# Performance work log

Measured on AMD Instinct MI355X. Metric: run time of the kernel, lower is better.

## Reference

```python
import jax, jax.numpy as jnp
import numpy as np

B, L, DIM = 1, 2048, 4096
H, KV, HD = 32, 8, 128
REP = H // KV
SCALE = HD ** -0.5
ROPE_BASE = 10000.0


def rope_traditional(x, offset=0):
    # x: [B, H, L, D] ; traditional RoPE rotates interleaved pairs (x[2i], x[2i+1])
    D = x.shape[-1]
    Lx = x.shape[2]
    pos = jnp.arange(offset, offset + Lx, dtype=jnp.float32)            # [L]
    inv_freq = ROPE_BASE ** (-jnp.arange(0, D, 2, dtype=jnp.float32) / D)  # [D/2]
    ang = pos[:, None] * inv_freq[None, :]                               # [L, D/2]
    c, s = jnp.cos(ang), jnp.sin(ang)
    x1 = x[..., 0::2]
    x2 = x[..., 1::2]
    r1 = x1 * c - x2 * s
    r2 = x1 * s + x2 * c
    return jnp.stack([r1, r2], axis=-1).reshape(x.shape).astype(x.dtype)


def setup_inputs() -> dict:
    key = jax.random.key(0)
    k0, k1, k2, k3, k4 = jax.random.split(key, 5)
    x = jax.random.normal(k0, (B, L, DIM), dtype=jnp.float32)
    wq = jax.random.normal(k1, (DIM, H * HD), dtype=jnp.float32) * 0.02
    wk = jax.random.normal(k2, (DIM, KV * HD), dtype=jnp.float32) * 0.02
    wv = jax.random.normal(k3, (DIM, KV * HD), dtype=jnp.float32) * 0.02
    wo = jax.random.normal(k4, (H * HD, DIM), dtype=jnp.float32) * 0.02
    # additive causal mask (prefill)
    causal = jnp.tril(jnp.ones((L, L), dtype=bool))
    mask = jnp.where(causal, 0.0, -1e9).astype(jnp.float32)
    return {"x": x, "wq": wq, "wk": wk, "wv": wv, "wo": wo, "mask": mask}


def reference(x, wq, wk, wv, wo, mask):
    Bx, Lx, _ = x.shape
    q = (x @ wq).reshape(Bx, Lx, H, HD).transpose(0, 2, 1, 3)   # [B,H,L,hd]
    k = (x @ wk).reshape(Bx, Lx, KV, HD).transpose(0, 2, 1, 3)  # [B,KV,L,hd]
    v = (x @ wv).reshape(Bx, Lx, KV, HD).transpose(0, 2, 1, 3)
    # GQA head repeat (each kv head repeated REP times contiguously)
    k = jnp.repeat(k, REP, axis=1)  # [B,H,L,hd]
    v = jnp.repeat(v, REP, axis=1)
    # RoPE applied after repeat (cache=None branch), offset 0
    q = rope_traditional(q)
    k = rope_traditional(k)
    scores = jnp.einsum("bhld,bhmd->bhlm", q * SCALE, k) + mask  # [B,H,L,L]
    probs = jax.nn.softmax(scores.astype(jnp.float32), axis=-1).astype(scores.dtype)
    out = jnp.einsum("bhlm,bhmd->bhld", probs, v)
    out = out.transpose(0, 2, 1, 3).reshape(Bx, Lx, H * HD)
    return out @ wo, k, v
```

## Files before the change

### kernel.cpp

```cpp
#include <hip/hip_runtime.h>
#include <hip/hip_bf16.h>
#include <math.h>


#define L_SEQ 2048
#define DIM   4096
#define NH    32
#define NKV   8
#define HD    128
#define SCALE 0.08838834764831845f

typedef __bf16 bf16x8 __attribute__((ext_vector_type(8)));
typedef __bf16 bf16x4 __attribute__((ext_vector_type(4)));
typedef __bf16 bf16x2 __attribute__((ext_vector_type(2)));
typedef float  f32x4  __attribute__((ext_vector_type(4)));

__device__ __forceinline__ void gld16(const void* g, void* l) {
  __builtin_amdgcn_global_load_lds(
      (const __attribute__((address_space(1))) void*)g,
      (__attribute__((address_space(3))) void*)l, 16, 0, 0);
}

__global__ void cast_bf16_kernel(const float* __restrict__ in,
                                 __bf16* __restrict__ out, long n4) {
  long i = blockIdx.x * (long)blockDim.x + threadIdx.x;
  if (i >= n4) return;
  float4 f = reinterpret_cast<const float4*>(in)[i];
  bf16x4 o;
  o[0] = (__bf16)f.x; o[1] = (__bf16)f.y; o[2] = (__bf16)f.z; o[3] = (__bf16)f.w;
  reinterpret_cast<bf16x4*>(out)[i] = o;
}

__global__ void tcast_kernel(const float* __restrict__ in0, __bf16* __restrict__ out0,
                             const float* __restrict__ in1, __bf16* __restrict__ out1,
                             int K, int N) {
  __shared__ float tile[32][33];
  const float* in  = blockIdx.z ? in1  : in0;
  __bf16*     out  = blockIdx.z ? out1 : out0;
  int n0 = blockIdx.x * 32, k0 = blockIdx.y * 32;
  int tx = threadIdx.x & 31, ty = threadIdx.x >> 5;
#pragma unroll
  for (int i = 0; i < 4; ++i)
    tile[ty + i * 8][tx] = in[(long)(k0 + ty + i * 8) * N + n0 + tx];
  __syncthreads();
#pragma unroll
  for (int i = 0; i < 4; ++i)
    out[(long)(n0 + ty + i * 8) * K + k0 + tx] = (__bf16)tile[tx][ty + i * 8];
}

template<int TN>
__global__ __launch_bounds__(512, 2) void gemm_t(
    const __bf16* __restrict__ A, const __bf16* __restrict__ B0,
    const __bf16* __restrict__ B1, void* __restrict__ C0, void* __restrict__ C1,
    int M, int N, int K, int mode) {
  constexpr int ABY = 128 * 64 * 2;
  constexpr int BBY = TN * 64 * 2;
  constexpr int BUF = ABY + BBY;
  __shared__ char lds[3 * BUF] __attribute__((aligned(16)));
  const __bf16* Bt = blockIdx.z ? B1 : B0;
  void* C = blockIdx.z ? C1 : C0;

  const int nwg = gridDim.x * gridDim.y;
  const int bid = blockIdx.y * gridDim.x + blockIdx.x;
  const int swz = (bid & 7) * (nwg >> 3) + (bid >> 3);
  const int n0 = (swz % gridDim.x) * TN;
  const int m0 = (swz / gridDim.x) * 128;

  const int t = threadIdx.x, wave = t >> 6, lane = t & 63;
  const int quad = lane >> 4, l16 = lane & 15;
  const int wm = (wave >> 2) * 64, wn = (wave & 3) * (TN / 4);

  const int srow = t >> 3;
  const int scol = ((t & 7) ^ (srow & 7)) * 8;
  const __bf16* pa = A  + (long)(m0 + srow) * K + scol;
  const __bf16* pb = Bt + (long)(n0 + srow) * K + scol;
  const long K64 = (long)64 * K;
  const int ldsA = wave * 1024;
  const int ldsB = ABY + wave * 1024;

  int aoff[2][4], boff[2][TN / 64];
#pragma unroll
  for (int ks = 0; ks < 2; ++ks) {
    const int sw = ((ks * 4 + quad) ^ (l16 & 7)) * 16;
#pragma unroll
    for (int i = 0; i < 4; ++i)
      aoff[ks][i] = (wm + i * 16 + l16) * 128 + sw;
#pragma unroll
    for (int i = 0; i < TN / 64; ++i)
      boff[ks][i] = ABY + (wn + i * 16 + l16) * 128 + sw;
  }

  f32x4 acc[4][TN / 64] = {};
  const int nt = K >> 6;

  {
    char* bb = lds;
#pragma unroll
    for (int pt = 0; pt < 2; ++pt) {
#pragma unroll
      for (int r = 0; r < 2; ++r) gld16(pa + r * K64, bb + ldsA + r * 8192);
#pragma unroll
      for (int r = 0; r < TN / 64; ++r) gld16(pb + r * K64, bb + ldsB + r * 8192);
      pa += 64; pb += 64;
      bb += BUF;
    }
  }

  char* cb = lds;
  char* sb = lds + 2 * BUF;

#pragma unroll 1
  for (int kt = 0; kt < nt - 1; ++kt) {
    if constexpr (TN == 256) asm volatile("s_waitcnt vmcnt(6)" ::: "memory");
    else                     asm volatile("s_waitcnt vmcnt(4)" ::: "memory");
    __builtin_amdgcn_s_barrier();
    bf16x8 af[4], bfr[TN / 64];
#pragma unroll
    for (int i = 0; i < 4; ++i) af[i] = *(const bf16x8*)(cb + aoff[0][i]);
#pragma unroll
    for (int i = 0; i < TN / 64; ++i) bfr[i] = *(const bf16x8*)(cb + boff[0][i]);
    if (kt + 2 < nt) {
#pragma unroll
      for (int r = 0; r < 2; ++r) gld16(pa + r * K64, sb + ldsA + r * 8192);
#pragma unroll
      for (int r = 0; r < TN / 64; ++r) gld16(pb + r * K64, sb + ldsB + r * 8192);
      pa += 64; pb += 64;
    }
    __builtin_amdgcn_s_setprio(1);
#pragma unroll
    for (int tm = 0; tm < 4; ++tm)
#pragma unroll
      for (int tn = 0; tn < TN / 64; ++tn)
        acc[tm][tn] = __builtin_amdgcn_mfma_f32_16x16x32_bf16(
            af[tm], bfr[tn], acc[tm][tn], 0, 0, 0);
    __builtin_amdgcn_s_setprio(0);
#pragma unroll
    for (int i = 0; i < 4; ++i) af[i] = *(const bf16x8*)(cb + aoff[1][i]);
#pragma unroll
    for (int i = 0; i < TN / 64; ++i) bfr[i] = *(const bf16x8*)(cb + boff[1][i]);
    __builtin_amdgcn_s_setprio(1);
#pragma unroll
    for (int tm = 0; tm < 4; ++tm)
#pragma unroll
      for (int tn = 0; tn < TN / 64; ++tn)
        acc[tm][tn] = __builtin_amdgcn_mfma_f32_16x16x32_bf16(
            af[tm], bfr[tn], acc[tm][tn], 0, 0, 0);
    __builtin_amdgcn_s_setprio(0);
    cb += BUF; if (cb == lds + 3 * BUF) cb = lds;
    sb += BUF; if (sb == lds + 3 * BUF) sb = lds;
  }

  asm volatile("s_waitcnt vmcnt(0)" ::: "memory");
  __builtin_amdgcn_s_barrier();
  {
    bf16x8 af[4], bfr[TN / 64];
#pragma unroll
    for (int ks = 0; ks < 2; ++ks) {
#pragma unroll
      for (int i = 0; i < 4; ++i) af[i] = *(const bf16x8*)(cb + aoff[ks][i]);
#pragma unroll
      for (int i = 0; i < TN / 64; ++i) bfr[i] = *(const bf16x8*)(cb + boff[ks][i]);
      __builtin_amdgcn_s_setprio(1);
#pragma unroll
      for (int tm = 0; tm < 4; ++tm)
#pragma unroll
        for (int tn = 0; tn < TN / 64; ++tn)
          acc[tm][tn] = __builtin_amdgcn_mfma_f32_16x16x32_bf16(
              af[tm], bfr[tn], acc[tm][tn], 0, 0, 0);
      __builtin_amdgcn_s_setprio(0);
    }
  }

#pragma unroll
  for (int tm = 0; tm < 4; ++tm)
#pragma unroll
    for (int tn = 0; tn < TN / 64; ++tn)
#pragma unroll
      for (int r = 0; r < 4; ++r) {
        int row = m0 + wm + tm * 16 + quad * 4 + r;
        int col = n0 + wn + tn * 16 + l16;
        float v = acc[tm][tn][r];
        if (mode == 0) {
          ((float*)C)[(long)row * N + col] = v;
        } else {
          long idx = ((long)(col >> 7) * L_SEQ + row) * HD + (col & 127);
          ((__bf16*)C)[idx] = (__bf16)v;
        }
      }
}

#define NLOG2_10K 13.287712379549449f

__global__ void rope_q_kernel(__bf16* __restrict__ q ) {
  int idx = blockIdx.x * blockDim.x + threadIdx.x;
  int i = idx & 63, l = (idx >> 6) & 2047, h = idx >> 17;
  if (h >= NH) return;
  long base = ((long)h * L_SEQ + l) * HD + 2 * i;
  bf16x2 x12 = *(bf16x2*)(q + base);
  float x1 = (float)x12[0], x2 = (float)x12[1];
  float inv = exp2f((float)i * (-NLOG2_10K / 64.0f));
  float s, c; __sincosf((float)l * inv, &s, &c);
  bf16x2 o; o[0] = (__bf16)(x1 * c - x2 * s); o[1] = (__bf16)(x1 * s + x2 * c);
  *(bf16x2*)(q + base) = o;
}

__global__ void ropekv_kernel(__bf16* __restrict__ kb ,
                              const __bf16* __restrict__ vb,
                              float* __restrict__ kout ,
                              float* __restrict__ vout) {
  int idx = blockIdx.x * blockDim.x + threadIdx.x;
  int i = idx & 63, l = (idx >> 6) & 2047, kv = idx >> 17;
  if (kv >= NKV) return;
  long base = ((long)kv * L_SEQ + l) * HD + 2 * i;
  bf16x2 x12 = *(bf16x2*)(kb + base);
  float x1 = (float)x12[0], x2 = (float)x12[1];
  float inv = exp2f((float)i * (-NLOG2_10K / 64.0f));
  float s, c; __sincosf((float)l * inv, &s, &c);
  float r1 = x1 * c - x2 * s, r2 = x1 * s + x2 * c;
  bf16x2 o; o[0] = (__bf16)r1; o[1] = (__bf16)r2;
  *(bf16x2*)(kb + base) = o;
  float2 kf; kf.x = r1; kf.y = r2;
  bf16x2 vv = *(const bf16x2*)(vb + base);
  float2 vf; vf.x = (float)vv[0]; vf.y = (float)vv[1];
  long off = (long)(kv * 4) * L_SEQ * HD + (long)l * HD + 2 * i;
#pragma unroll
  for (int rr = 0; rr < 4; ++rr) {
    *(float2*)(kout + off) = kf;
    *(float2*)(vout + off) = vf;
    off += (long)L_SEQ * HD;
  }
}

__global__ void vtrans_kernel(const __bf16* __restrict__ Vh, __bf16* __restrict__ Vt) {
  __shared__ __bf16 tile[64 * 65];
  int kv = blockIdx.z, lb = blockIdx.x * 64, db = blockIdx.y * 64;
  int t = threadIdx.x;
#pragma unroll
  for (int it = 0; it < 2; ++it) {
    int c = it * 256 + t, r = c >> 3, pc = c & 7;
    bf16x8 v = *(const bf16x8*)(Vh + ((long)kv * L_SEQ + lb + r) * HD + db + pc * 8);
#pragma unroll
    for (int e = 0; e < 8; ++e) tile[r * 65 + pc * 8 + e] = v[e];
  }
  __syncthreads();
#pragma unroll
  for (int it = 0; it < 2; ++it) {
    int c = it * 256 + t, r = c >> 3, pc = c & 7;
    bf16x8 v;
#pragma unroll
    for (int e = 0; e < 8; ++e) v[e] = tile[(pc * 8 + e) * 65 + r];
    *(bf16x8*)(Vt + ((long)kv * HD + db + r) * L_SEQ + lb + pc * 8) = v;
  }
}

#define DTHR 8.0f

__global__ __launch_bounds__(256, 2) void attn5_kernel(
    const __bf16* __restrict__ Q, const __bf16* __restrict__ K,
    const __bf16* __restrict__ Vt, __bf16* __restrict__ O ) {
  __shared__ __bf16 Ks[2][64 * 128]  __attribute__((aligned(16)));
  __shared__ __bf16 Vts[128 * 64]    __attribute__((aligned(16)));
  __shared__ __bf16 Ps[128 * 64]     __attribute__((aligned(16)));

  const int b = blockIdx.x;
  const int kvg = b & 7;
  const int h   = kvg * 4 + ((b >> 3) & 3);
  const int i16 = b >> 5;
  const int qt  = (i16 < 8) ? (15 - i16) : (i16 - 8);
  const int t = threadIdx.x, wave = t >> 6, lane = t & 63;
  const int quad = lane >> 4, l16 = lane & 15;
  const int mw = wave * 32;
  const __bf16* Kh = K  + (long)kvg * L_SEQ * HD;
  const __bf16* Vh = Vt + (long)kvg * HD * L_SEQ;
  const float SL2 = SCALE * 1.44269504f;

  int kr[4], kk[4], vr[4], vk[4];
#pragma unroll
  for (int it = 0; it < 4; ++it) {
    int c = it * 256 + t;
    kr[it] = c >> 4; kk[it] = ((c & 15) ^ (kr[it] & 7)) * 8;
    vr[it] = c >> 3; vk[it] = ((c & 7)  ^ (vr[it] & 7)) * 8;
  }

  const int nchunk = 2 * qt + 2;
  const int jdiag  = 2 * qt;

  int mq[2]; mq[0] = qt * 128 + mw + l16; mq[1] = mq[0] + 16;

  bf16x8 bq[2][4];
#pragma unroll
  for (int g = 0; g < 2; ++g) {
    const __bf16* qrow = Q + ((long)h * L_SEQ + mq[g]) * HD + quad * 8;
#pragma unroll
    for (int d = 0; d < 4; ++d) bq[g][d] = *(const bf16x8*)(qrow + d * 32);
  }

  f32x4 o_acc[2][8] = {};
  float m_run[2] = {-1e30f, -1e30f}, l_run[2] = {0.f, 0.f};

#pragma unroll
  for (int it = 0; it < 4; ++it)
    gld16(Kh + (long)kr[it] * HD + kk[it],
          (char*)Ks[0] + (size_t)(it * 256 + wave * 64) * 16);

#pragma unroll 1
  for (int j = 0; j < nchunk; ++j) {
    const int kcur = j & 1;
    asm volatile("s_waitcnt vmcnt(0)" ::: "memory");
    __builtin_amdgcn_s_barrier();

#pragma unroll
    for (int it = 0; it < 4; ++it)
      gld16(Vh + (long)vr[it] * L_SEQ + j * 64 + vk[it],
            (char*)Vts + (size_t)(it * 256 + wave * 64) * 16);
    if (j + 1 < nchunk) {
#pragma unroll
      for (int it = 0; it < 4; ++it)
        gld16(Kh + (long)((j + 1) * 64 + kr[it]) * HD + kk[it],
              (char*)Ks[kcur ^ 1] + (size_t)(it * 256 + wave * 64) * 16);
    }

    f32x4 s[2][4] = {};
    __builtin_amdgcn_s_setprio(1);
#pragma unroll
    for (int dsi = 0; dsi < 4; ++dsi)
#pragma unroll
      for (int tn = 0; tn < 4; ++tn) {
        bf16x8 ak = *(const bf16x8*)((char*)Ks[kcur] + (tn * 16 + l16) * 256 +
                                     (((dsi * 4 + quad) ^ (l16 & 7)) * 16));
        s[0][tn] = __builtin_amdgcn_mfma_f32_16x16x32_bf16(ak, bq[0][dsi], s[0][tn], 0, 0, 0);
        s[1][tn] = __builtin_amdgcn_mfma_f32_16x16x32_bf16(ak, bq[1][dsi], s[1][tn], 0, 0, 0);
      }
    __builtin_amdgcn_s_setprio(0);

#pragma unroll
    for (int g = 0; g < 2; ++g) {
#pragma unroll
      for (int tn = 0; tn < 4; ++tn)
#pragma unroll
        for (int r = 0; r < 4; ++r) {
          float v = s[g][tn][r] * SL2;
          if (j >= jdiag && (j * 64 + tn * 16 + quad * 4 + r) > mq[g]) v = -3.0e38f;
          s[g][tn][r] = v;
        }
      float mx = -3.0e38f;
#pragma unroll
      for (int tn = 0; tn < 4; ++tn)
#pragma unroll
        for (int r = 0; r < 4; ++r) mx = fmaxf(mx, s[g][tn][r]);
      mx = fmaxf(mx, __shfl_xor(mx, 16, 64));
      mx = fmaxf(mx, __shfl_xor(mx, 32, 64));

      const bool defer = __all(mx - m_run[g] <= DTHR);
      const float mnew = defer ? m_run[g] : fmaxf(m_run[g], mx);

      float rs = 0.f;
#pragma unroll
      for (int tn = 0; tn < 4; ++tn)
#pragma unroll
        for (int r = 0; r < 4; ++r) {
          float pe = exp2f(s[g][tn][r] - mnew);
          s[g][tn][r] = pe; rs += pe;
        }
      rs += __shfl_xor(rs, 16, 64);
      rs += __shfl_xor(rs, 32, 64);

      if (defer) {
        l_run[g] += rs;
      } else {
        float alpha = exp2f(m_run[g] - mnew);
#pragma unroll
        for (int td = 0; td < 8; ++td)
#pragma unroll
          for (int r = 0; r < 4; ++r) o_acc[g][td][r] *= alpha;
        l_run[g] = l_run[g] * alpha + rs;
        m_run[g] = mnew;
      }

#pragma unroll
      for (int tn = 0; tn < 4; ++tn) {
        bf16x4 pv;
#pragma unroll
        for (int r = 0; r < 4; ++r) pv[r] = (__bf16)s[g][tn][r];
        *(bf16x4*)((char*)Ps + (mw + g * 16 + l16) * 128 +
                   ((tn * 32 + quad * 8) ^ ((l16 & 7) << 4))) = pv;
      }
    }

    if (j + 1 < nchunk) asm volatile("s_waitcnt vmcnt(4)" ::: "memory");
    else                asm volatile("s_waitcnt vmcnt(0)" ::: "memory");
    __builtin_amdgcn_s_barrier();

    __builtin_amdgcn_s_setprio(1);
#pragma unroll
    for (int ks = 0; ks < 2; ++ks) {
      bf16x8 bp0 = *(const bf16x8*)((char*)Ps + (mw + l16) * 128 +
                                    ((ks * 64 + quad * 16) ^ ((l16 & 7) << 4)));
      bf16x8 bp1 = *(const bf16x8*)((char*)Ps + (mw + 16 + l16) * 128 +
                                    ((ks * 64 + quad * 16) ^ ((l16 & 7) << 4)));
#pragma unroll
      for (int td = 0; td < 8; ++td) {
        bf16x8 av = *(const bf16x8*)((char*)Vts + (td * 16 + l16) * 128 +
                                     (((ks * 4 + quad) ^ (l16 & 7)) * 16));
        o_acc[0][td] = __builtin_amdgcn_mfma_f32_16x16x32_bf16(av, bp0, o_acc[0][td], 0, 0, 0);
        o_acc[1][td] = __builtin_amdgcn_mfma_f32_16x16x32_bf16(av, bp1, o_acc[1][td], 0, 0, 0);
      }
    }
    __builtin_amdgcn_s_setprio(0);
  }

#pragma unroll
  for (int g = 0; g < 2; ++g) {
    float inv_l = 1.0f / l_run[g];
#pragma unroll
    for (int td = 0; td < 8; ++td) {
      bf16x4 ov;
#pragma unroll
      for (int r = 0; r < 4; ++r) ov[r] = (__bf16)(o_acc[g][td][r] * inv_l);
      *(bf16x4*)(O + (long)mq[g] * DIM + h * HD + td * 16 + quad * 4) = ov;
    }
  }
}

extern "C" void kernel_launch(void* const* d_in, const int* in_sizes, int n_in,
                              void* d_out, int out_size, void* d_ws, size_t ws_size,
                              hipStream_t stream) {
  const float* x  = (const float*)d_in[0];
  const float* wq = (const float*)d_in[1];
  const float* wk = (const float*)d_in[2];
  const float* wv = (const float*)d_in[3];
  const float* wo = (const float*)d_in[4];

  float* out   = (float*)d_out;
  float* k_out = out + (long)L_SEQ * DIM;
  float* v_out = k_out + (long)NH * L_SEQ * HD;

  char* ws = (char*)d_ws;
  __bf16* Xb  = (__bf16*)ws; ws += (long)L_SEQ * DIM * 2;
  __bf16* Wqt = (__bf16*)ws; ws += (long)DIM * DIM * 2;
  __bf16* Wkt = (__bf16*)ws; ws += (long)DIM * (NKV * HD) * 2;
  __bf16* Wvt = (__bf16*)ws; ws += (long)DIM * (NKV * HD) * 2;
  __bf16* Wot = (__bf16*)ws; ws += (long)DIM * DIM * 2;
  __bf16* Qh  = (__bf16*)ws; ws += (long)NH * L_SEQ * HD * 2;
  __bf16* Kh  = (__bf16*)ws; ws += (long)NKV * L_SEQ * HD * 2;
  __bf16* Vh  = (__bf16*)ws; ws += (long)NKV * L_SEQ * HD * 2;
  __bf16* Vt  = (__bf16*)ws; ws += (long)NKV * HD * L_SEQ * 2;
  __bf16* Ob  = (__bf16*)ws; ws += (long)L_SEQ * DIM * 2;

  tcast_kernel<<<dim3(DIM / 32, DIM / 32, 1), 256, 0, stream>>>(wq, Wqt, wq, Wqt, DIM, DIM);
  tcast_kernel<<<dim3((NKV * HD) / 32, DIM / 32, 2), 256, 0, stream>>>(wk, Wkt, wv, Wvt, DIM, NKV * HD);
  tcast_kernel<<<dim3(DIM / 32, DIM / 32, 1), 256, 0, stream>>>(wo, Wot, wo, Wot, DIM, DIM);
  {
    long n = (long)L_SEQ * DIM;
    cast_bf16_kernel<<<dim3(n / 1024), 256, 0, stream>>>(x, Xb, n / 4);
  }
  gemm_t<256><<<dim3(DIM / 256, L_SEQ / 128, 1), 512, 0, stream>>>(
      Xb, Wqt, Wqt, Qh, Qh, L_SEQ, DIM, DIM, 2);
  gemm_t<128><<<dim3((NKV * HD) / 128, L_SEQ / 128, 2), 512, 0, stream>>>(
      Xb, Wkt, Wvt, Kh, Vh, L_SEQ, NKV * HD, DIM, 2);
  rope_q_kernel<<<dim3((NH * L_SEQ * 64) / 256), 256, 0, stream>>>(Qh);
  ropekv_kernel<<<dim3((NKV * L_SEQ * 64) / 256), 256, 0, stream>>>(Kh, Vh, k_out, v_out);
  vtrans_kernel<<<dim3(L_SEQ / 64, HD / 64, NKV), 256, 0, stream>>>(Vh, Vt);
  attn5_kernel<<<dim3(512), 256, 0, stream>>>(Qh, Kh, Vt, Ob);
  gemm_t<256><<<dim3(DIM / 256, L_SEQ / 128, 1), 512, 0, stream>>>(
      Ob, Wot, Wot, out, out, L_SEQ, DIM, DIM, 0);
}
```

Before: 548.7 us.

## Split attention work across 8 waves with 16 query rows each

The attention kernel now launches 512 threads (8 waves) per block instead of 256. Each wave handles 16 query rows instead of 32, so per-wave registers for S, O accumulators and softmax state are halved, and each thread issues half as many K/V tile loads. The aim is more waves in flight to hide latency and a lighter register footprint. In exchange, each K fragment read from LDS now feeds one MFMA instead of two, and barriers must synchronise more waves.

Result: faster. 524.4 us (-4.4%).

```diff
diff --git a/kernel.cpp b/kernel.cpp
--- a/kernel.cpp
+++ b/kernel.cpp
@@ -255,7 +255,7 @@
 
 #define DTHR 8.0f
 
-__global__ __launch_bounds__(256, 2) void attn5_kernel(
+__global__ __launch_bounds__(512, 4) void attn6_kernel(
     const __bf16* __restrict__ Q, const __bf16* __restrict__ K,
     const __bf16* __restrict__ Vt, __bf16* __restrict__ O ) {
   __shared__ __bf16 Ks[2][64 * 128]  __attribute__((aligned(16)));
@@ -269,15 +269,15 @@
   const int qt  = (i16 < 8) ? (15 - i16) : (i16 - 8);
   const int t = threadIdx.x, wave = t >> 6, lane = t & 63;
   const int quad = lane >> 4, l16 = lane & 15;
-  const int mw = wave * 32;
+  const int mw = wave * 16;
   const __bf16* Kh = K  + (long)kvg * L_SEQ * HD;
   const __bf16* Vh = Vt + (long)kvg * HD * L_SEQ;
   const float SL2 = SCALE * 1.44269504f;
 
-  int kr[4], kk[4], vr[4], vk[4];
-#pragma unroll
-  for (int it = 0; it < 4; ++it) {
-    int c = it * 256 + t;
+  int kr[2], kk[2], vr[2], vk[2];
+#pragma unroll
+  for (int it = 0; it < 2; ++it) {
+    int c = it * 512 + t;
     kr[it] = c >> 4; kk[it] = ((c & 15) ^ (kr[it] & 7)) * 8;
     vr[it] = c >> 3; vk[it] = ((c & 7)  ^ (vr[it] & 7)) * 8;
   }
@@ -285,23 +285,22 @@
   const int nchunk = 2 * qt + 2;
   const int jdiag  = 2 * qt;
 
-  int mq[2]; mq[0] = qt * 128 + mw + l16; mq[1] = mq[0] + 16;
-
-  bf16x8 bq[2][4];
-#pragma unroll
-  for (int g = 0; g < 2; ++g) {
-    const __bf16* qrow = Q + ((long)h * L_SEQ + mq[g]) * HD + quad * 8;
-#pragma unroll
-    for (int d = 0; d < 4; ++d) bq[g][d] = *(const bf16x8*)(qrow + d * 32);
-  }
-
-  f32x4 o_acc[2][8] = {};
-  float m_run[2] = {-1e30f, -1e30f}, l_run[2] = {0.f, 0.f};
-
-#pragma unroll
-  for (int it = 0; it < 4; ++it)
+  const int mq = qt * 128 + mw + l16;
+
+  bf16x8 bq[4];
+  {
+    const __bf16* qrow = Q + ((long)h * L_SEQ + mq) * HD + quad * 8;
+#pragma unroll
+    for (int d = 0; d < 4; ++d) bq[d] = *(const bf16x8*)(qrow + d * 32);
+  }
+
+  f32x4 o_acc[8] = {};
+  float m_run = -1e30f, l_run = 0.f;
+
+#pragma unroll
+  for (int it = 0; it < 2; ++it)
     gld16(Kh + (long)kr[it] * HD + kk[it],
-          (char*)Ks[0] + (size_t)(it * 256 + wave * 64) * 16);
+          (char*)Ks[0] + (size_t)(it * 512 + wave * 64) * 16);
 
 #pragma unroll 1
   for (int j = 0; j < nchunk; ++j) {
@@ -310,17 +309,17 @@
     __builtin_amdgcn_s_barrier();
 
 #pragma unroll
-    for (int it = 0; it < 4; ++it)
+    for (int it = 0; it < 2; ++it)
       gld16(Vh + (long)vr[it] * L_SEQ + j * 64 + vk[it],
-            (char*)Vts + (size_t)(it * 256 + wave * 64) * 16);
+            (char*)Vts + (size_t)(it * 512 + wave * 64) * 16);
     if (j + 1 < nchunk) {
 #pragma unroll
-      for (int it = 0; it < 4; ++it)
+      for (int it = 0; it < 2; ++it)
         gld16(Kh + (long)((j + 1) * 64 + kr[it]) * HD + kk[it],
-              (char*)Ks[kcur ^ 1] + (size_t)(it * 256 + wave * 64) * 16);
-    }
-
-    f32x4 s[2][4] = {};
+              (char*)Ks[kcur ^ 1] + (size_t)(it * 512 + wave * 64) * 16);
+    }
+
+    f32x4 s[4] = {};
     __builtin_amdgcn_s_setprio(1);
 #pragma unroll
     for (int dsi = 0; dsi < 4; ++dsi)
@@ -328,97 +327,87 @@
       for (int tn = 0; tn < 4; ++tn) {
         bf16x8 ak = *(const bf16x8*)((char*)Ks[kcur] + (tn * 16 + l16) * 256 +
                                      (((dsi * 4 + quad) ^ (l16 & 7)) * 16));
-        s[0][tn] = __builtin_amdgcn_mfma_f32_16x16x32_bf16(ak, bq[0][dsi], s[0][tn], 0, 0, 0);
-        s[1][tn] = __builtin_amdgcn_mfma_f32_16x16x32_bf16(ak, bq[1][dsi], s[1][tn], 0, 0, 0);
+        s[tn] = __builtin_amdgcn_mfma_f32_16x16x32_bf16(ak, bq[dsi], s[tn], 0, 0, 0);
       }
     __builtin_amdgcn_s_setprio(0);
 
 #pragma unroll
-    for (int g = 0; g < 2; ++g) {
-#pragma unroll
-      for (int tn = 0; tn < 4; ++tn)
-#pragma unroll
-        for (int r = 0; r < 4; ++r) {
-          float v = s[g][tn][r] * SL2;
-          if (j >= jdiag && (j * 64 + tn * 16 + quad * 4 + r) > mq[g]) v = -3.0e38f;
-          s[g][tn][r] = v;
-        }
-      float mx = -3.0e38f;
-#pragma unroll
-      for (int tn = 0; tn < 4; ++tn)
-#pragma unroll
-        for (int r = 0; r < 4; ++r) mx = fmaxf(mx, s[g][tn][r]);
-      mx = fmaxf(mx, __shfl_xor(mx, 16, 64));
-      mx = fmaxf(mx, __shfl_xor(mx, 32, 64));
-
-      const bool defer = __all(mx - m_run[g] <= DTHR);
-      const float mnew = defer ? m_run[g] : fmaxf(m_run[g], mx);
-
-      float rs = 0.f;
-#pragma unroll
-      for (int tn = 0; tn < 4; ++tn)
-#pragma unroll
-        for (int r = 0; r < 4; ++r) {
-          float pe = exp2f(s[g][tn][r] - mnew);
-          s[g][tn][r] = pe; rs += pe;
-        }
-      rs += __shfl_xor(rs, 16, 64);
-      rs += __shfl_xor(rs, 32, 64);
-
-      if (defer) {
-        l_run[g] += rs;
-      } else {
-        float alpha = exp2f(m_run[g] - mnew);
-#pragma unroll
-        for (int td = 0; td < 8; ++td)
-#pragma unroll
-          for (int r = 0; r < 4; ++r) o_acc[g][td][r] *= alpha;
-        l_run[g] = l_run[g] * alpha + rs;
-        m_run[g] = mnew;
+    for (int tn = 0; tn < 4; ++tn)
+#pragma unroll
+      for (int r = 0; r < 4; ++r) {
+        float v = s[tn][r] * SL2;
+        if (j >= jdiag && (j * 64 + tn * 16 + quad * 4 + r) > mq) v = -3.0e38f;
+        s[tn][r] = v;
       }
-
-#pragma unroll
-      for (int tn = 0; tn < 4; ++tn) {
-        bf16x4 pv;
-#pragma unroll
-        for (int r = 0; r < 4; ++r) pv[r] = (__bf16)s[g][tn][r];
-        *(bf16x4*)((char*)Ps + (mw + g * 16 + l16) * 128 +
-                   ((tn * 32 + quad * 8) ^ ((l16 & 7) << 4))) = pv;
+    float mx = -3.0e38f;
+#pragma unroll
+    for (int tn = 0; tn < 4; ++tn)
+#pragma unroll
+      for (int r = 0; r < 4; ++r) mx = fmaxf(mx, s[tn][r]);
+    mx = fmaxf(mx, __shfl_xor(mx, 16, 64));
+    mx = fmaxf(mx, __shfl_xor(mx, 32, 64));
+
+    const bool defer = __all(mx - m_run <= DTHR);
+    const float mnew = defer ? m_run : fmaxf(m_run, mx);
+
+    float rs = 0.f;
+#pragma unroll
+    for (int tn = 0; tn < 4; ++tn)
+#pragma unroll
+      for (int r = 0; r < 4; ++r) {
+        float pe = exp2f(s[tn][r] - mnew);
+        s[tn][r] = pe; rs += pe;
       }
-    }
-
-    if (j + 1 < nchunk) asm volatile("s_waitcnt vmcnt(4)" ::: "memory");
+    rs += __shfl_xor(rs, 16, 64);
+    rs += __shfl_xor(rs, 32, 64);
+
+    if (defer) {
+      l_run += rs;
+    } else {
+      float alpha = exp2f(m_run - mnew);
+#pragma unroll
+      for (int td = 0; td < 8; ++td)
+#pragma unroll
+        for (int r = 0; r < 4; ++r) o_acc[td][r] *= alpha;
+      l_run = l_run * alpha + rs;
+      m_run = mnew;
+    }
+
+#pragma unroll
+    for (int tn = 0; tn < 4; ++tn) {
+      bf16x4 pv;
+#pragma unroll
+      for (int r = 0; r < 4; ++r) pv[r] = (__bf16)s[tn][r];
+      *(bf16x4*)((char*)Ps + (mw + l16) * 128 +
+                 ((tn * 32 + quad * 8) ^ ((l16 & 7) << 4))) = pv;
+    }
+
+    if (j + 1 < nchunk) asm volatile("s_waitcnt vmcnt(2)" ::: "memory");
     else                asm volatile("s_waitcnt vmcnt(0)" ::: "memory");
     __builtin_amdgcn_s_barrier();
 
     __builtin_amdgcn_s_setprio(1);
 #pragma unroll
     for (int ks = 0; ks < 2; ++ks) {
-      bf16x8 bp0 = *(const bf16x8*)((char*)Ps + (mw + l16) * 128 +
-                                    ((ks * 64 + quad * 16) ^ ((l16 & 7) << 4)));
-      bf16x8 bp1 = *(const bf16x8*)((char*)Ps + (mw + 16 + l16) * 128 +
-                                    ((ks * 64 + quad * 16) ^ ((l16 & 7) << 4)));
+      bf16x8 bp = *(const bf16x8*)((char*)Ps + (mw + l16) * 128 +
+                                   ((ks * 64 + quad * 16) ^ ((l16 & 7) << 4)));
 #pragma unroll
       for (int td = 0; td < 8; ++td) {
         bf16x8 av = *(const bf16x8*)((char*)Vts + (td * 16 + l16) * 128 +
                                      (((ks * 4 + quad) ^ (l16 & 7)) * 16));
-        o_acc[0][td] = __builtin_amdgcn_mfma_f32_16x16x32_bf16(av, bp0, o_acc[0][td], 0, 0, 0);
-        o_acc[1][td] = __builtin_amdgcn_mfma_f32_16x16x32_bf16(av, bp1, o_acc[1][td], 0, 0, 0);
+        o_acc[td] = __builtin_amdgcn_mfma_f32_16x16x32_bf16(av, bp, o_acc[td], 0, 0, 0);
       }
     }
     __builtin_amdgcn_s_setprio(0);
   }
 
-#pragma unroll
-  for (int g = 0; g < 2; ++g) {
-    float inv_l = 1.0f / l_run[g];
-#pragma unroll
-    for (int td = 0; td < 8; ++td) {
-      bf16x4 ov;
-#pragma unroll
-      for (int r = 0; r < 4; ++r) ov[r] = (__bf16)(o_acc[g][td][r] * inv_l);
-      *(bf16x4*)(O + (long)mq[g] * DIM + h * HD + td * 16 + quad * 4) = ov;
-    }
+  float inv_l = 1.0f / l_run;
+#pragma unroll
+  for (int td = 0; td < 8; ++td) {
+    bf16x4 ov;
+#pragma unroll
+    for (int r = 0; r < 4; ++r) ov[r] = (__bf16)(o_acc[td][r] * inv_l);
+    *(bf16x4*)(O + (long)mq * DIM + h * HD + td * 16 + quad * 4) = ov;
   }
 }
 
@@ -461,7 +450,7 @@
   rope_q_kernel<<<dim3((NH * L_SEQ * 64) / 256), 256, 0, stream>>>(Qh);
   ropekv_kernel<<<dim3((NKV * L_SEQ * 64) / 256), 256, 0, stream>>>(Kh, Vh, k_out, v_out);
   vtrans_kernel<<<dim3(L_SEQ / 64, HD / 64, NKV), 256, 0, stream>>>(Vh, Vt);
-  attn5_kernel<<<dim3(512), 256, 0, stream>>>(Qh, Kh, Vt, Ob);
+  attn6_kernel<<<dim3(512), 512, 0, stream>>>(Qh, Kh, Vt, Ob);
   gemm_t<256><<<dim3(DIM / 256, L_SEQ / 128, 1), 512, 0, stream>>>(
       Ob, Wot, Wot, out, out, L_SEQ, DIM, DIM, 0);
 }
```
